# Kernel optimization log

Hardware: AMD Instinct MI355X
Metric: run time of the kernel (lower is better)

Reference implementation:

```python
import jax, jax.numpy as jnp
import numpy as np

BS, S, D, H, DFF, L = 8, 1024, 256, 8, 1024, 3
DK = D // H
NEG = -1e32


def setup_inputs() -> dict:
    key = jax.random.key(0)
    ks = jax.random.split(key, 10)
    r = lambda k, shp: jax.random.normal(k, shp, jnp.float32) * 0.02
    return {
        "q_embed_data": jax.random.normal(ks[0], (BS, S, D), jnp.float32),
        "qa_embed_data": jax.random.normal(ks[1], (BS, S, D), jnp.float32),
        "Wk": r(ks[2], (L, D, D)), "bk": jnp.zeros((L, D), jnp.float32),
        "Wv": r(ks[3], (L, D, D)), "bv": jnp.zeros((L, D), jnp.float32),
        "Wo": r(ks[4], (L, D, D)), "bo": jnp.zeros((L, D), jnp.float32),
        "gammas": r(ks[5], (L, H)),
        "ln1_g": jnp.ones((L, D), jnp.float32), "ln1_b": jnp.zeros((L, D), jnp.float32),
        "W1": r(ks[6], (L, D, DFF)), "b1": jnp.zeros((L, DFF), jnp.float32),
        "W2": r(ks[7], (L, DFF, D)), "b2": jnp.zeros((L, D), jnp.float32),
        "ln2_g": jnp.ones((L, D), jnp.float32), "ln2_b": jnp.zeros((L, D), jnp.float32),
    }


def _layernorm(x, g, b, eps=1e-5):
    mu = x.mean(-1, keepdims=True)
    var = ((x - mu) ** 2).mean(-1, keepdims=True)
    return (x - mu) * jax.lax.rsqrt(var + eps) * g + b


def _attn(xq, xk, xv, Wk, bk, Wv, bv, Wo, bo, gamma, mask, zero_pad):
    # kq_same=1: q and k both use k_linear
    bs = xq.shape[0]
    q = (xq @ Wk + bk).reshape(bs, S, H, DK).transpose(0, 2, 1, 3)  # bhsd
    k = (xk @ Wk + bk).reshape(bs, S, H, DK).transpose(0, 2, 1, 3)
    v = (xv @ Wv + bv).reshape(bs, S, H, DK).transpose(0, 2, 1, 3)
    scores = jnp.einsum('bhid,bhjd->bhij', q, k) / np.float32(np.sqrt(DK))
    mf = mask.astype(scores.dtype)
    # no-grad decay branch (detached in torch)
    p = jax.nn.softmax(jnp.where(mask, scores, NEG), axis=-1) * mf
    distcum = jnp.cumsum(p, axis=-1)
    disttot = p.sum(axis=-1, keepdims=True)
    idx = jnp.arange(S)
    pos = jnp.abs(idx[None, :] - idx[:, None]).astype(jnp.float32)[None, None]
    dist = jnp.sqrt(jnp.clip((disttot - distcum) * pos, 0.0, None))
    dist = jax.lax.stop_gradient(dist)
    g = -jax.nn.softplus(gamma)[None, :, None, None]  # (1,H,1,1)
    total_effect = jnp.clip(jnp.exp(dist * g), 1e-5, 1e5)
    scores = scores * total_effect
    attn = jax.nn.softmax(jnp.where(mask, scores, NEG), axis=-1)
    if zero_pad:
        attn = attn.at[:, :, 0, :].set(0.0)
    out = jnp.einsum('bhij,bhjd->bhid', attn, v)
    out = out.transpose(0, 2, 1, 3).reshape(bs, S, D)
    return out @ Wo + bo


def _block(i, xq, xk, xv, mask, zero_pad, apply_pos, P):
    Wk, bk, Wv, bv, Wo, bo, gam, l1g, l1b, W1, b1, W2, b2, l2g, l2b = [p[i] for p in P]
    q2 = _attn(xq, xk, xv, Wk, bk, Wv, bv, Wo, bo, gam, mask, zero_pad)
    x = _layernorm(xq + q2, l1g, l1b)
    if apply_pos:
        ff = jax.nn.relu(x @ W1 + b1) @ W2 + b2
        x = _layernorm(x + ff, l2g, l2b)
    return x


def _forward(q_embed_data, qa_embed_data, Wk, bk, Wv, bv, Wo, bo, gammas,
             ln1_g, ln1_b, W1, b1, W2, b2, ln2_g, ln2_b):
    P = (Wk, bk, Wv, bv, Wo, bo, gammas, ln1_g, ln1_b, W1, b1, W2, b2, ln2_g, ln2_b)
    tri_incl = jnp.tril(jnp.ones((S, S), bool))[None, None]       # mask=1: peek current+past
    tri_excl = jnp.tril(jnp.ones((S, S), bool), -1)[None, None]   # mask=0: strictly past
    x, y = q_embed_data, qa_embed_data
    # blocks_1 (n_blocks=1): mask=1, apply_pos=True, self-attn on y
    y = _block(0, y, y, y, tri_incl, False, True, P)
    # blocks_2 (2*n_blocks=2): alternate (mask=1, no FFN) / (mask=0, zero_pad, FFN, values=y)
    x = _block(1, x, x, x, tri_incl, False, False, P)
    x = _block(2, x, x, y, tri_excl, True, True, P)
    return x


def reference(q_embed_data, qa_embed_data, Wk, bk, Wv, bv, Wo, bo, gammas,
              ln1_g, ln1_b, W1, b1, W2, b2, ln2_g, ln2_b):
    return _forward(q_embed_data, qa_embed_data, Wk, bk, Wv, bv, Wo, bo, gammas,
                    ln1_g, ln1_b, W1, b1, W2, b2, ln2_g, ln2_b)
```

## Files before the change

### kernel.cpp

```cpp
#include <hip/hip_runtime.h>

typedef unsigned short u16;
typedef float f32x4 __attribute__((ext_vector_type(4)));
typedef __bf16 bf16x8 __attribute__((ext_vector_type(8)));
typedef u16 u16x8 __attribute__((ext_vector_type(8)));
typedef u16 u16x4 __attribute__((ext_vector_type(4)));

__device__ __forceinline__ u16 f2bf(float f) {
  union { float f; unsigned u; } v; v.f = f;
  unsigned r = (v.u + 0x7FFFu + ((v.u >> 16) & 1u)) >> 16;
  return (u16)r;
}
__device__ __forceinline__ float bf2f(u16 h) {
  union { unsigned u; float f; } v; v.u = ((unsigned)h) << 16;
  return v.f;
}
__device__ __forceinline__ unsigned cvtpk_bf16(float lo, float hi) {
  unsigned r;
  asm("v_cvt_pk_bf16_f32 %0, %1, %2" : "=v"(r) : "v"(lo), "v"(hi));
  return r;
}
__device__ __forceinline__ float wred_sum(float v) {
#pragma unroll
  for (int o = 32; o >= 1; o >>= 1) v += __shfl_xor(v, o);
  return v;
}

template <int RELU, int WF32, int WBF, int WVT>
__global__ __launch_bounds__(256) void gemm_kernel(
    const u16* __restrict__ A, const u16* __restrict__ Bt,
    const float* __restrict__ bias, float* __restrict__ C,
    u16* __restrict__ Cbf, int M, int N, int K) {
  __shared__ u16 As[64 * 64];
  __shared__ u16 Bs[64 * 64];
  const int tid = threadIdx.x;
  const int lane = tid & 63;
  const int w = tid >> 6;
  const int m0 = blockIdx.x * 64;
  const int n0 = blockIdx.y * 64;
  const int wr = (w >> 1) * 32;
  const int wc = (w & 1) * 32;
  const int l15 = lane & 15, hi = lane >> 4;

  f32x4 acc[2][2] = {};

  for (int k0 = 0; k0 < K; k0 += 64) {
#pragma unroll
    for (int rep = 0; rep < 2; ++rep) {
      int idx = tid + rep * 256;
      int row = idx >> 3, c8 = idx & 7;
      int cs = ((c8 ^ (row & 7)) << 3);
      __builtin_amdgcn_global_load_lds(
          (const __attribute__((address_space(1))) void*)(A + (size_t)(m0 + row) * K + k0 + cs),
          (__attribute__((address_space(3))) void*)(&As[idx * 8]), 16, 0, 0);
      __builtin_amdgcn_global_load_lds(
          (const __attribute__((address_space(1))) void*)(Bt + (size_t)(n0 + row) * K + k0 + cs),
          (__attribute__((address_space(3))) void*)(&Bs[idx * 8]), 16, 0, 0);
    }
    __syncthreads();
#pragma unroll
    for (int kk = 0; kk < 2; ++kk) {
      int kb = (kk * 32 + (hi << 3)) << 1;
      bf16x8 af[2], bfr[2];
#pragma unroll
      for (int mf = 0; mf < 2; ++mf) {
        int m = wr + mf * 16 + l15;
        af[mf] = *(const bf16x8*)((const char*)As + m * 128 + (kb ^ ((m & 7) << 4)));
      }
#pragma unroll
      for (int nf = 0; nf < 2; ++nf) {
        int n = wc + nf * 16 + l15;
        bfr[nf] = *(const bf16x8*)((const char*)Bs + n * 128 + (kb ^ ((n & 7) << 4)));
      }
#pragma unroll
      for (int mf = 0; mf < 2; ++mf)
#pragma unroll
        for (int nf = 0; nf < 2; ++nf)
          acc[mf][nf] = __builtin_amdgcn_mfma_f32_16x16x32_bf16(af[mf], bfr[nf], acc[mf][nf], 0, 0, 0);
    }
    __syncthreads();
  }

#pragma unroll
  for (int mf = 0; mf < 2; ++mf)
#pragma unroll
    for (int nf = 0; nf < 2; ++nf) {
      int col = n0 + wc + nf * 16 + l15;
      float bia = bias[col];
      u16x4 tv;
#pragma unroll
      for (int r = 0; r < 4; ++r) {
        int row = m0 + wr + mf * 16 + (hi << 2) + r;
        float val = acc[mf][nf][r] + bia;
        if (RELU) val = fmaxf(val, 0.f);
        if (WF32) C[(size_t)row * N + col] = val;
        if (WBF) Cbf[(size_t)row * N + col] = f2bf(val);
        if (WVT) tv[r] = f2bf(val);
      }
      if (WVT) {
        int row0 = m0 + wr + mf * 16 + (hi << 2);
        size_t addr = (((size_t)(row0 >> 10) * 8 + (col >> 5)) * 32 + (col & 31)) * 1024 + (row0 & 1023);
        *(u16x4*)(Cbf + addr) = tv;
      }
    }
}

template <int RELU>
__global__ __launch_bounds__(256) void gemm_w_kernel(
    const u16* __restrict__ A, const u16* __restrict__ Bt,
    const float* __restrict__ bias, u16* __restrict__ Cbf,
    int M, int N, int K) {
  __shared__ u16 As[64 * 64];
  __shared__ u16 Bs[128 * 64];
  const int tid = threadIdx.x;
  const int lane = tid & 63;
  const int w = tid >> 6;
  const int m0 = blockIdx.x * 64;
  const int n0 = blockIdx.y * 128;
  const int wr = (w >> 1) * 32;
  const int wc = (w & 1) * 64;
  const int l15 = lane & 15, hi = lane >> 4;

  f32x4 acc[2][4] = {};

  for (int k0 = 0; k0 < K; k0 += 64) {
#pragma unroll
    for (int rep = 0; rep < 2; ++rep) {
      int idx = tid + rep * 256;
      int row = idx >> 3, c8 = idx & 7;
      int cs = ((c8 ^ (row & 7)) << 3);
      __builtin_amdgcn_global_load_lds(
          (const __attribute__((address_space(1))) void*)(A + (size_t)(m0 + row) * K + k0 + cs),
          (__attribute__((address_space(3))) void*)(&As[idx * 8]), 16, 0, 0);
    }
#pragma unroll
    for (int rep = 0; rep < 4; ++rep) {
      int idx = tid + rep * 256;
      int row = idx >> 3, c8 = idx & 7;
      int cs = ((c8 ^ (row & 7)) << 3);
      __builtin_amdgcn_global_load_lds(
          (const __attribute__((address_space(1))) void*)(Bt + (size_t)(n0 + row) * K + k0 + cs),
          (__attribute__((address_space(3))) void*)(&Bs[idx * 8]), 16, 0, 0);
    }
    __syncthreads();
#pragma unroll
    for (int kk = 0; kk < 2; ++kk) {
      int kb = (kk * 32 + (hi << 3)) << 1;
      bf16x8 af[2], bfr[4];
#pragma unroll
      for (int mf = 0; mf < 2; ++mf) {
        int m = wr + mf * 16 + l15;
        af[mf] = *(const bf16x8*)((const char*)As + m * 128 + (kb ^ ((m & 7) << 4)));
      }
#pragma unroll
      for (int nf = 0; nf < 4; ++nf) {
        int n = wc + nf * 16 + l15;
        bfr[nf] = *(const bf16x8*)((const char*)Bs + n * 128 + (kb ^ ((n & 7) << 4)));
      }
#pragma unroll
      for (int mf = 0; mf < 2; ++mf)
#pragma unroll
        for (int nf = 0; nf < 4; ++nf)
          acc[mf][nf] = __builtin_amdgcn_mfma_f32_16x16x32_bf16(af[mf], bfr[nf], acc[mf][nf], 0, 0, 0);
    }
    __syncthreads();
  }

#pragma unroll
  for (int mf = 0; mf < 2; ++mf)
#pragma unroll
    for (int nf = 0; nf < 4; ++nf) {
      int col = n0 + wc + nf * 16 + l15;
      float bia = bias[col];
#pragma unroll
      for (int r = 0; r < 4; ++r) {
        int row = m0 + wr + mf * 16 + (hi << 2) + r;
        float val = acc[mf][nf][r] + bia;
        if (RELU) val = fmaxf(val, 0.f);
        Cbf[(size_t)row * N + col] = f2bf(val);
      }
    }
}

__global__ __launch_bounds__(256) void gemm_kv_kernel(
    const u16* __restrict__ A, const u16* __restrict__ Bt,
    const float* __restrict__ biasK, const float* __restrict__ biasV,
    u16* __restrict__ qkbf, u16* __restrict__ vT, int M, int N, int K) {
  __shared__ u16 As[64 * 64];
  __shared__ u16 Bs[128 * 64];
  const int tid = threadIdx.x;
  const int lane = tid & 63;
  const int w = tid >> 6;
  const int m0 = blockIdx.x * 64;
  const int n0 = blockIdx.y * 128;
  const int wr = (w >> 1) * 32;
  const int wc = (w & 1) * 64;
  const int l15 = lane & 15, hi = lane >> 4;

  f32x4 acc[2][4] = {};

  for (int k0 = 0; k0 < K; k0 += 64) {
#pragma unroll
    for (int rep = 0; rep < 2; ++rep) {
      int idx = tid + rep * 256;
      int row = idx >> 3, c8 = idx & 7;
      int cs = ((c8 ^ (row & 7)) << 3);
      __builtin_amdgcn_global_load_lds(
          (const __attribute__((address_space(1))) void*)(A + (size_t)(m0 + row) * K + k0 + cs),
          (__attribute__((address_space(3))) void*)(&As[idx * 8]), 16, 0, 0);
    }
#pragma unroll
    for (int rep = 0; rep < 4; ++rep) {
      int idx = tid + rep * 256;
      int row = idx >> 3, c8 = idx & 7;
      int cs = ((c8 ^ (row & 7)) << 3);
      __builtin_amdgcn_global_load_lds(
          (const __attribute__((address_space(1))) void*)(Bt + (size_t)(n0 + row) * K + k0 + cs),
          (__attribute__((address_space(3))) void*)(&Bs[idx * 8]), 16, 0, 0);
    }
    __syncthreads();
#pragma unroll
    for (int kk = 0; kk < 2; ++kk) {
      int kb = (kk * 32 + (hi << 3)) << 1;
      bf16x8 af[2], bfr[4];
#pragma unroll
      for (int mf = 0; mf < 2; ++mf) {
        int m = wr + mf * 16 + l15;
        af[mf] = *(const bf16x8*)((const char*)As + m * 128 + (kb ^ ((m & 7) << 4)));
      }
#pragma unroll
      for (int nf = 0; nf < 4; ++nf) {
        int n = wc + nf * 16 + l15;
        bfr[nf] = *(const bf16x8*)((const char*)Bs + n * 128 + (kb ^ ((n & 7) << 4)));
      }
#pragma unroll
      for (int mf = 0; mf < 2; ++mf)
#pragma unroll
        for (int nf = 0; nf < 4; ++nf)
          acc[mf][nf] = __builtin_amdgcn_mfma_f32_16x16x32_bf16(af[mf], bfr[nf], acc[mf][nf], 0, 0, 0);
    }
    __syncthreads();
  }

#pragma unroll
  for (int mf = 0; mf < 2; ++mf)
#pragma unroll
    for (int nf = 0; nf < 4; ++nf) {
      int col = n0 + wc + nf * 16 + l15;
      const bool isV = (col >= 256);
      float bia = isV ? biasV[col - 256] : biasK[col];
      u16x4 tv;
#pragma unroll
      for (int r = 0; r < 4; ++r) {
        int row = m0 + wr + mf * 16 + (hi << 2) + r;
        float val = acc[mf][nf][r] + bia;
        if (!isV) qkbf[(size_t)row * 256 + col] = f2bf(val);
        tv[r] = f2bf(val);
      }
      if (isV) {
        int row0 = m0 + wr + mf * 16 + (hi << 2);
        int vc = col - 256;
        size_t addr = (((size_t)(row0 >> 10) * 8 + (vc >> 5)) * 32 + (vc & 31)) * 1024 + (row0 & 1023);
        *(u16x4*)(vT + addr) = tv;
      }
    }
}

__global__ __launch_bounds__(256) void attn_mfma_kernel(
    const u16* __restrict__ qkbf, const u16* __restrict__ vT,
    u16* __restrict__ ao, const float* __restrict__ gam, int excl) {
  __shared__ float zbuf[4][16];
  __shared__ float z2buf[4][16];
  __shared__ float accbuf[8][4][64];

  const int lane = threadIdx.x & 63, w = threadIdx.x >> 6;
  const int qt = 63 - blockIdx.y;
  const int bh = blockIdx.x;
  const int b = bh >> 3, h = bh & 7;
  const int q0 = qt * 16;
  const int l15 = lane & 15, hi = lane >> 4;
  const int i = q0 + l15;
  const float LOG2E = 1.4426950408889634f;
  const float g2 = -log1pf(__expf(gam[h])) * LOG2E;
  const float cscale = 0.17677669529663687f * LOG2E;
  const float CLIP2 = -16.609640474436812f;

  const u16* kbase = qkbf + (size_t)b * 1024 * 256 + h * 32;
  const u16* vbase = vT + (size_t)bh * 32 * 1024;
  const bf16x8 qfrag = *(const bf16x8*)(kbase + (size_t)i * 256 + hi * 8);

  const int mylim = i - excl;
  const int jmax = q0 + 15 - excl;
  const int ntiles = (jmax >> 4) + 1;
  const int C = (ntiles + 3) >> 2;
  const int c0 = w * C;
  const int tEnd = (c0 + C < ntiles) ? (c0 + C) : ntiles;
  const int count = (tEnd > c0) ? (tEnd - c0) : 0;

  auto calc_l = [&](int t, float* l) {
    bf16x8 kf = *(const bf16x8*)(kbase + (size_t)(t * 16 + l15) * 256 + hi * 8);
    f32x4 sA = {};
    sA = __builtin_amdgcn_mfma_f32_16x16x32_bf16(kf, qfrag, sA, 0, 0, 0);
    l[0] = sA[0] * cscale; l[1] = sA[1] * cscale;
    l[2] = sA[2] * cscale; l[3] = sA[3] * cscale;
    if (t == ntiles - 1) {
      const int kb = t * 16 + hi * 4;
      l[0] = (kb + 0 <= mylim) ? l[0] : -1000.f;
      l[1] = (kb + 1 <= mylim) ? l[1] : -1000.f;
      l[2] = (kb + 2 <= mylim) ? l[2] : -1000.f;
      l[3] = (kb + 3 <= mylim) ? l[3] : -1000.f;
    }
  };

  float zacc = 0.f;
  for (int t = c0; t < tEnd; ++t) {
    float l[4]; calc_l(t, l);
    zacc += (exp2f(l[0]) + exp2f(l[1])) + (exp2f(l[2]) + exp2f(l[3]));
  }
  zacc += __shfl_xor(zacc, 16);
  zacc += __shfl_xor(zacc, 32);
  if (lane < 16) zbuf[w][lane] = zacc;
  __syncthreads();

  const float zc0 = zbuf[0][l15], zc1 = zbuf[1][l15];
  const float zc2 = zbuf[2][l15], zc3 = zbuf[3][l15];
  const float Z = zc0 + zc1 + zc2 + zc3;
  const float invZ = Z > 0.f ? 1.f / Z : 0.f;
  float prefix = 0.f;
  if (w > 0) prefix += zc0;
  if (w > 1) prefix += zc1;
  if (w > 2) prefix += zc2;

  float carry = prefix, z2 = 0.f;
  f32x4 acc0 = {}, acc1 = {};

  auto sm4 = [&](const float* l, int kb) -> uint2 {
    const float e0 = exp2f(l[0]), e1 = exp2f(l[1]);
    const float e2 = exp2f(l[2]), e3 = exp2f(l[3]);
    const float cA = e0 + e1, cB2 = cA + e2, cC = cB2 + e3;
    float vsc = cC;
    float tmp = __shfl_up(vsc, 16); if (hi >= 1) vsc += tmp;
    tmp = __shfl_up(vsc, 32); if (hi >= 2) vsc += tmp;
    const float exg = vsc - cC;
    const float tot = __shfl(vsc, l15 + 48);
    const float cb = carry + exg;
    carry += tot;
    const float posb = (float)(i - kb);
    const float r0 = (Z - (cb + e0)) * invZ;
    const float r1 = (Z - (cb + cA)) * invZ;
    const float r2 = (Z - (cb + cB2)) * invZ;
    const float r3 = (Z - (cb + cC)) * invZ;
    const float d20 = fmaxf(r0 * posb, 0.f);
    const float d21 = fmaxf(r1 * (posb - 1.f), 0.f);
    const float d22 = fmaxf(r2 * (posb - 2.f), 0.f);
    const float d23 = fmaxf(r3 * (posb - 3.f), 0.f);
    const float a0 = fmaxf(__builtin_amdgcn_sqrtf(d20) * g2, CLIP2);
    const float a1 = fmaxf(__builtin_amdgcn_sqrtf(d21) * g2, CLIP2);
    const float a2 = fmaxf(__builtin_amdgcn_sqrtf(d22) * g2, CLIP2);
    const float a3 = fmaxf(__builtin_amdgcn_sqrtf(d23) * g2, CLIP2);
    const float p0 = exp2f(l[0] * exp2f(a0));
    const float p1 = exp2f(l[1] * exp2f(a1));
    const float p2 = exp2f(l[2] * exp2f(a2));
    const float p3 = exp2f(l[3] * exp2f(a3));
    z2 += (p0 + p1) + (p2 + p3);
    uint2 r; r.x = cvtpk_bf16(p0, p1); r.y = cvtpk_bf16(p2, p3);
    return r;
  };

  const int Cp = (count + 1) & ~1;
  for (int tl = 0; tl < Cp; tl += 2) {
    const int t0 = c0 + tl, t1 = t0 + 1;
    float la[4], lb[4];
    calc_l(t0, la);
    const bool v1 = (tl + 1 < count);
    if (v1) calc_l(t1, lb);
    const int jb = t0 * 16;
    bf16x8 vf0 = *(const bf16x8*)(vbase + (size_t)l15 * 1024 + jb + hi * 8);
    bf16x8 vf1 = *(const bf16x8*)(vbase + (size_t)(16 + l15) * 1024 + jb + hi * 8);
    uint2 uA = sm4(la, t0 * 16 + hi * 4);
    uint2 uB = make_uint2(0u, 0u);
    if (v1) uB = sm4(lb, t1 * 16 + hi * 4);
    const int srcA = l15 + (((2 * hi) & 3) << 4);
    const int srcB = l15 + (((2 * hi + 1) & 3) << 4);
    unsigned a00 = (unsigned)__shfl((int)uA.x, srcA);
    unsigned a01 = (unsigned)__shfl((int)uB.x, srcA);
    unsigned a10 = (unsigned)__shfl((int)uA.y, srcA);
    unsigned a11 = (unsigned)__shfl((int)uB.y, srcA);
    unsigned b00 = (unsigned)__shfl((int)uA.x, srcB);
    unsigned b01 = (unsigned)__shfl((int)uB.x, srcB);
    unsigned b10 = (unsigned)__shfl((int)uA.y, srcB);
    unsigned b11 = (unsigned)__shfl((int)uB.y, srcB);
    const bool up = hi >= 2;
    union { unsigned u[4]; bf16x8 v; } pf;
    pf.u[0] = up ? a01 : a00;
    pf.u[1] = up ? a11 : a10;
    pf.u[2] = up ? b01 : b00;
    pf.u[3] = up ? b11 : b10;
    acc0 = __builtin_amdgcn_mfma_f32_16x16x32_bf16(vf0, pf.v, acc0, 0, 0, 0);
    acc1 = __builtin_amdgcn_mfma_f32_16x16x32_bf16(vf1, pf.v, acc1, 0, 0, 0);
  }

  z2 += __shfl_xor(z2, 16);
  z2 += __shfl_xor(z2, 32);
  if (lane < 16) z2buf[w][lane] = z2;
#pragma unroll
  for (int j = 0; j < 4; ++j) {
    accbuf[j][w][lane] = acc0[j];
    accbuf[4 + j][w][lane] = acc1[j];
  }
  __syncthreads();

  if (w == 0) {
    const float z2t = z2buf[0][l15] + z2buf[1][l15] + z2buf[2][l15] + z2buf[3][l15];
    const float inv2 = z2t > 0.f ? 1.f / z2t : 0.f;
    u16* aop = ao + ((size_t)(b * 1024 + i)) * 256 + h * 32;
    float s0[4], s1[4];
#pragma unroll
    for (int j = 0; j < 4; ++j) {
      s0[j] = (accbuf[j][0][lane] + accbuf[j][1][lane] + accbuf[j][2][lane] + accbuf[j][3][lane]) * inv2;
      s1[j] = (accbuf[4 + j][0][lane] + accbuf[4 + j][1][lane] + accbuf[4 + j][2][lane] + accbuf[4 + j][3][lane]) * inv2;
    }
    uint2 o0, o1;
    o0.x = cvtpk_bf16(s0[0], s0[1]); o0.y = cvtpk_bf16(s0[2], s0[3]);
    o1.x = cvtpk_bf16(s1[0], s1[1]); o1.y = cvtpk_bf16(s1[2], s1[3]);
    *(uint2*)(aop + hi * 4) = o0;
    *(uint2*)(aop + 16 + hi * 4) = o1;
  }
}

__global__ __launch_bounds__(256) void add_ln_kernel(
    const float* __restrict__ res, const u16* __restrict__ add,
    const float* __restrict__ g, const float* __restrict__ b,
    float* __restrict__ outf, u16* __restrict__ outb) {
  const int lane = threadIdx.x & 63, wid = threadIdx.x >> 6;
  const size_t row = (size_t)blockIdx.x * 4 + wid;
  const size_t base = row * 256 + lane * 4;
  float4 rv = *(const float4*)(res + base);
  u16x4 av = *(const u16x4*)(add + base);
  float x0 = rv.x + bf2f(av[0]), x1 = rv.y + bf2f(av[1]);
  float x2 = rv.z + bf2f(av[2]), x3 = rv.w + bf2f(av[3]);
  float sm = wred_sum(x0 + x1 + x2 + x3);
  float mu = sm * (1.f / 256.f);
  float d0 = x0 - mu, d1 = x1 - mu, d2 = x2 - mu, d3 = x3 - mu;
  float vs = wred_sum(d0 * d0 + d1 * d1 + d2 * d2 + d3 * d3);
  float rs = rsqrtf(vs * (1.f / 256.f) + 1e-5f);
  float4 gv = *(const float4*)(g + lane * 4);
  float4 bv = *(const float4*)(b + lane * 4);
  float o0 = d0 * rs * gv.x + bv.x;
  float o1 = d1 * rs * gv.y + bv.y;
  float o2 = d2 * rs * gv.z + bv.z;
  float o3 = d3 * rs * gv.w + bv.w;
  float4 ov = {o0, o1, o2, o3};
  *(float4*)(outf + base) = ov;
  u16x4 wv; wv[0] = f2bf(o0); wv[1] = f2bf(o1); wv[2] = f2bf(o2); wv[3] = f2bf(o3);
  *(u16x4*)(outb + base) = wv;
}

__global__ __launch_bounds__(256) void cast_bf_kernel(
    const float* __restrict__ in, u16* __restrict__ out) {
  size_t i = ((size_t)blockIdx.x * 256 + threadIdx.x) * 8;
  float4 a = *(const float4*)(in + i);
  float4 c = *(const float4*)(in + i + 4);
  u16x8 o;
  o[0] = f2bf(a.x); o[1] = f2bf(a.y); o[2] = f2bf(a.z); o[3] = f2bf(a.w);
  o[4] = f2bf(c.x); o[5] = f2bf(c.y); o[6] = f2bf(c.z); o[7] = f2bf(c.w);
  *(u16x8*)(out + i) = o;
}

__global__ __launch_bounds__(256) void transpose_cast_kernel(
    const float* __restrict__ W, u16* __restrict__ Wt, int K, int N,
    int dstStride) {
  __shared__ float t[32][33];
  const size_t lo = (size_t)blockIdx.z * K * N;
  const size_t lod = (size_t)blockIdx.z * dstStride;
  int n0 = blockIdx.x * 32, k0 = blockIdx.y * 32;
  int tx = threadIdx.x, ty = threadIdx.y;
#pragma unroll
  for (int r = 0; r < 32; r += 8)
    t[ty + r][tx] = W[lo + (size_t)(k0 + ty + r) * N + n0 + tx];
  __syncthreads();
#pragma unroll
  for (int r = 0; r < 32; r += 8)
    Wt[lod + (size_t)(n0 + ty + r) * K + k0 + tx] = f2bf(t[tx][ty + r]);
}

extern "C" void kernel_launch(void* const* d_in, const int* in_sizes, int n_in,
                              void* d_out, int out_size, void* d_ws,
                              size_t ws_size, hipStream_t stream) {
  const float* q_embed = (const float*)d_in[0];
  const float* qa_embed = (const float*)d_in[1];
  const float* Wk = (const float*)d_in[2];
  const float* bk = (const float*)d_in[3];
  const float* Wv = (const float*)d_in[4];
  const float* bv = (const float*)d_in[5];
  const float* Wo = (const float*)d_in[6];
  const float* bo = (const float*)d_in[7];
  const float* gammas = (const float*)d_in[8];
  const float* ln1_g = (const float*)d_in[9];
  const float* ln1_b = (const float*)d_in[10];
  const float* W1 = (const float*)d_in[11];
  const float* b1 = (const float*)d_in[12];
  const float* W2 = (const float*)d_in[13];
  const float* b2 = (const float*)d_in[14];
  const float* ln2_g = (const float*)d_in[15];
  const float* ln2_b = (const float*)d_in[16];

  const size_t ACT_F32 = (size_t)8192 * 256 * 4;
  const size_t ACT_BF = (size_t)8192 * 256 * 2;
  char* p = (char*)d_ws;
  auto carve = [&](size_t bytes) {
    void* r = (void*)p;
    p += (bytes + 255) & ~(size_t)255;
    return r;
  };
  float* yb = (float*)carve(ACT_F32);
  float* xb = (float*)carve(ACT_F32);
  u16* pofb = (u16*)carve(ACT_BF);
  u16* xbf = (u16*)carve(ACT_BF);
  u16* ybf = (u16*)carve(ACT_BF);
  u16* qkbf = (u16*)carve(ACT_BF);
  u16* vTb = (u16*)carve(ACT_BF);
  u16* aobf = (u16*)carve(ACT_BF);
  u16* hbf = (u16*)carve((size_t)8192 * 1024 * 2);
  u16* Wkvt = (u16*)carve((size_t)3 * 131072 * 2);
  u16* Wot = (u16*)carve((size_t)3 * 65536 * 2);
  u16* W1t = (u16*)carve((size_t)3 * 262144 * 2);
  u16* W2t = (u16*)carve((size_t)3 * 262144 * 2);

  dim3 tb(32, 8);
  transpose_cast_kernel<<<dim3(8, 8, 3), tb, 0, stream>>>(Wk, Wkvt, 256, 256, 131072);
  transpose_cast_kernel<<<dim3(8, 8, 3), tb, 0, stream>>>(Wv, Wkvt + 65536, 256, 256, 131072);
  transpose_cast_kernel<<<dim3(8, 8, 3), tb, 0, stream>>>(Wo, Wot, 256, 256, 65536);
  transpose_cast_kernel<<<dim3(32, 8, 3), tb, 0, stream>>>(W1, W1t, 256, 1024, 262144);
  transpose_cast_kernel<<<dim3(8, 32, 3), tb, 0, stream>>>(W2, W2t, 1024, 256, 262144);
  cast_bf_kernel<<<1024, 256, 0, stream>>>(q_embed, xbf);
  cast_bf_kernel<<<1024, 256, 0, stream>>>(qa_embed, ybf);

  const dim3 gP(128, 4), gKV(128, 4), gW1(128, 8);
  const dim3 gA(64, 64);

  gemm_kv_kernel<<<gKV, 256, 0, stream>>>(ybf, Wkvt, bk, bv, qkbf, vTb, 8192, 512, 256);
  attn_mfma_kernel<<<gA, 256, 0, stream>>>(qkbf, vTb, aobf, gammas, 0);
  gemm_kernel<0, 0, 1, 0><<<gP, 256, 0, stream>>>(aobf, Wot, bo, nullptr, pofb, 8192, 256, 256);
  add_ln_kernel<<<2048, 256, 0, stream>>>(qa_embed, pofb, ln1_g, ln1_b, yb, ybf);
  gemm_w_kernel<1><<<gW1, 256, 0, stream>>>(ybf, W1t, b1, hbf, 8192, 1024, 256);
  gemm_kernel<0, 0, 1, 0><<<gP, 256, 0, stream>>>(hbf, W2t, b2, nullptr, pofb, 8192, 256, 1024);
  add_ln_kernel<<<2048, 256, 0, stream>>>(yb, pofb, ln2_g, ln2_b, yb, ybf);

  gemm_kv_kernel<<<gKV, 256, 0, stream>>>(xbf, Wkvt + 131072, bk + 256, bv + 256, qkbf, vTb, 8192, 512, 256);
  attn_mfma_kernel<<<gA, 256, 0, stream>>>(qkbf, vTb, aobf, gammas + 8, 0);
  gemm_kernel<0, 0, 1, 0><<<gP, 256, 0, stream>>>(aobf, Wot + 65536, bo + 256, nullptr, pofb, 8192, 256, 256);
  add_ln_kernel<<<2048, 256, 0, stream>>>(q_embed, pofb, ln1_g + 256, ln1_b + 256, xb, xbf);

  gemm_kv_kernel<<<gKV, 256, 0, stream>>>(xbf, Wkvt + 262144, bk + 512, bv + 512, qkbf, vTb, 8192, 512, 256);
  gemm_kernel<0, 0, 0, 1><<<gP, 256, 0, stream>>>(ybf, Wkvt + 262144 + 65536, bv + 512, nullptr, vTb, 8192, 256, 256);
  attn_mfma_kernel<<<gA, 256, 0, stream>>>(qkbf, vTb, aobf, gammas + 16, 1);
  gemm_kernel<0, 0, 1, 0><<<gP, 256, 0, stream>>>(aobf, Wot + 131072, bo + 512, nullptr, pofb, 8192, 256, 256);
  add_ln_kernel<<<2048, 256, 0, stream>>>(xb, pofb, ln1_g + 512, ln1_b + 512, xb, xbf);
  gemm_w_kernel<1><<<gW1, 256, 0, stream>>>(xbf, W1t + 524288, b1 + 2048, hbf, 8192, 1024, 256);
  gemm_kernel<0, 0, 1, 0><<<gP, 256, 0, stream>>>(hbf, W2t + 524288, b2 + 512, nullptr, pofb, 8192, 256, 1024);
  add_ln_kernel<<<2048, 256, 0, stream>>>(xb, pofb, ln2_g + 512, ln2_b + 512, (float*)d_out, xbf);
}
```

Measured before the change: 313.7 us.

## Fuse output/FFN2 GEMMs with residual add and LayerNorm; merge prep kernels

Adds a gemm_ln kernel that computes a full 256-wide output row tile (32 rows per block) so the residual add and LayerNorm run in the GEMM epilogue. This removes the bf16 intermediate buffer round trip and the separate add_ln launches. The seven weight transpose/cast and embedding cast launches are merged into one prep kernel. The trade-offs are that each fused GEMM launches only 256 blocks with a large B tile in LDS, which may lower occupancy, and that variance is now computed as E[x^2]-mu^2 in a single pass.

```diff
diff --git a/kernel.cpp b/kernel.cpp
--- a/kernel.cpp
+++ b/kernel.cpp
@@ -11,26 +11,15 @@
   unsigned r = (v.u + 0x7FFFu + ((v.u >> 16) & 1u)) >> 16;
   return (u16)r;
 }
-__device__ __forceinline__ float bf2f(u16 h) {
-  union { unsigned u; float f; } v; v.u = ((unsigned)h) << 16;
-  return v.f;
-}
 __device__ __forceinline__ unsigned cvtpk_bf16(float lo, float hi) {
   unsigned r;
   asm("v_cvt_pk_bf16_f32 %0, %1, %2" : "=v"(r) : "v"(lo), "v"(hi));
   return r;
 }
-__device__ __forceinline__ float wred_sum(float v) {
-#pragma unroll
-  for (int o = 32; o >= 1; o >>= 1) v += __shfl_xor(v, o);
-  return v;
-}
-
-template <int RELU, int WF32, int WBF, int WVT>
-__global__ __launch_bounds__(256) void gemm_kernel(
+
+__global__ __launch_bounds__(256) void gemm_vt_kernel(
     const u16* __restrict__ A, const u16* __restrict__ Bt,
-    const float* __restrict__ bias, float* __restrict__ C,
-    u16* __restrict__ Cbf, int M, int N, int K) {
+    const float* __restrict__ bias, u16* __restrict__ vT, int M, int N, int K) {
   __shared__ u16 As[64 * 64];
   __shared__ u16 Bs[64 * 64];
   const int tid = threadIdx.x;
@@ -90,18 +79,12 @@
       u16x4 tv;
 #pragma unroll
       for (int r = 0; r < 4; ++r) {
-        int row = m0 + wr + mf * 16 + (hi << 2) + r;
         float val = acc[mf][nf][r] + bia;
-        if (RELU) val = fmaxf(val, 0.f);
-        if (WF32) C[(size_t)row * N + col] = val;
-        if (WBF) Cbf[(size_t)row * N + col] = f2bf(val);
-        if (WVT) tv[r] = f2bf(val);
-      }
-      if (WVT) {
-        int row0 = m0 + wr + mf * 16 + (hi << 2);
-        size_t addr = (((size_t)(row0 >> 10) * 8 + (col >> 5)) * 32 + (col & 31)) * 1024 + (row0 & 1023);
-        *(u16x4*)(Cbf + addr) = tv;
-      }
+        tv[r] = f2bf(val);
+      }
+      int row0 = m0 + wr + mf * 16 + (hi << 2);
+      size_t addr = (((size_t)(row0 >> 10) * 8 + (col >> 5)) * 32 + (col & 31)) * 1024 + (row0 & 1023);
+      *(u16x4*)(vT + addr) = tv;
     }
 }
 
@@ -264,6 +247,114 @@
         *(u16x4*)(vT + addr) = tv;
       }
     }
+}
+
+__global__ __launch_bounds__(256) void gemm_ln_kernel(
+    const u16* __restrict__ A, const u16* __restrict__ Bt,
+    const float* __restrict__ bias, const float* __restrict__ res,
+    const float* __restrict__ g, const float* __restrict__ b,
+    float* __restrict__ outf, u16* __restrict__ outb, int K) {
+  __shared__ u16 As[32 * 64];
+  __shared__ u16 Bs[256 * 64];
+  __shared__ float red[2][32][2];
+
+  const int tid = threadIdx.x;
+  const int lane = tid & 63;
+  const int w = tid >> 6;
+  const int rowgrp = w >> 1, colh = w & 1;
+  const int m0 = blockIdx.x * 32;
+  const int l15 = lane & 15, hi = lane >> 4;
+
+  f32x4 acc[8] = {};
+
+  for (int k0 = 0; k0 < K; k0 += 64) {
+    {
+      int row = tid >> 3, c8 = tid & 7;
+      int cs = ((c8 ^ (row & 7)) << 3);
+      __builtin_amdgcn_global_load_lds(
+          (const __attribute__((address_space(1))) void*)(A + (size_t)(m0 + row) * K + k0 + cs),
+          (__attribute__((address_space(3))) void*)(&As[tid * 8]), 16, 0, 0);
+    }
+#pragma unroll
+    for (int rep = 0; rep < 8; ++rep) {
+      int idx = tid + rep * 256;
+      int row = idx >> 3, c8 = idx & 7;
+      int cs = ((c8 ^ (row & 7)) << 3);
+      __builtin_amdgcn_global_load_lds(
+          (const __attribute__((address_space(1))) void*)(Bt + (size_t)row * K + k0 + cs),
+          (__attribute__((address_space(3))) void*)(&Bs[idx * 8]), 16, 0, 0);
+    }
+    __syncthreads();
+#pragma unroll
+    for (int kk = 0; kk < 2; ++kk) {
+      int kb = (kk * 32 + (hi << 3)) << 1;
+      int m = rowgrp * 16 + l15;
+      bf16x8 af = *(const bf16x8*)((const char*)As + m * 128 + (kb ^ ((m & 7) << 4)));
+      bf16x8 bfr[8];
+#pragma unroll
+      for (int nf = 0; nf < 8; ++nf) {
+        int n = colh * 128 + nf * 16 + l15;
+        bfr[nf] = *(const bf16x8*)((const char*)Bs + n * 128 + (kb ^ ((n & 7) << 4)));
+      }
+#pragma unroll
+      for (int nf = 0; nf < 8; ++nf)
+        acc[nf] = __builtin_amdgcn_mfma_f32_16x16x32_bf16(af, bfr[nf], acc[nf], 0, 0, 0);
+    }
+    __syncthreads();
+  }
+
+  const int rbase = m0 + rowgrp * 16 + hi * 4;
+  float s[4] = {0.f, 0.f, 0.f, 0.f}, ss[4] = {0.f, 0.f, 0.f, 0.f};
+#pragma unroll
+  for (int nf = 0; nf < 8; ++nf) {
+    int col = colh * 128 + nf * 16 + l15;
+    float bia = bias[col];
+#pragma unroll
+    for (int r = 0; r < 4; ++r) {
+      float v = acc[nf][r] + bia + res[(size_t)(rbase + r) * 256 + col];
+      acc[nf][r] = v;
+      s[r] += v;
+      ss[r] += v * v;
+    }
+  }
+#pragma unroll
+  for (int r = 0; r < 4; ++r) {
+#pragma unroll
+    for (int o = 1; o < 16; o <<= 1) {
+      s[r] += __shfl_xor(s[r], o);
+      ss[r] += __shfl_xor(ss[r], o);
+    }
+  }
+  if (l15 == 0) {
+#pragma unroll
+    for (int r = 0; r < 4; ++r) {
+      red[colh][rowgrp * 16 + hi * 4 + r][0] = s[r];
+      red[colh][rowgrp * 16 + hi * 4 + r][1] = ss[r];
+    }
+  }
+  __syncthreads();
+  float mu[4], rs[4];
+#pragma unroll
+  for (int r = 0; r < 4; ++r) {
+    int rr = rowgrp * 16 + hi * 4 + r;
+    float S = red[0][rr][0] + red[1][rr][0];
+    float SS = red[0][rr][1] + red[1][rr][1];
+    mu[r] = S * (1.f / 256.f);
+    float var = SS * (1.f / 256.f) - mu[r] * mu[r];
+    rs[r] = rsqrtf(var + 1e-5f);
+  }
+#pragma unroll
+  for (int nf = 0; nf < 8; ++nf) {
+    int col = colh * 128 + nf * 16 + l15;
+    float gv = g[col], bv = b[col];
+#pragma unroll
+    for (int r = 0; r < 4; ++r) {
+      float o = (acc[nf][r] - mu[r]) * rs[r] * gv + bv;
+      size_t addr = (size_t)(rbase + r) * 256 + col;
+      outf[addr] = o;
+      outb[addr] = f2bf(o);
+    }
+  }
 }
 
 __global__ __launch_bounds__(256) void attn_mfma_kernel(
@@ -428,60 +519,63 @@
   }
 }
 
-__global__ __launch_bounds__(256) void add_ln_kernel(
-    const float* __restrict__ res, const u16* __restrict__ add,
-    const float* __restrict__ g, const float* __restrict__ b,
-    float* __restrict__ outf, u16* __restrict__ outb) {
-  const int lane = threadIdx.x & 63, wid = threadIdx.x >> 6;
-  const size_t row = (size_t)blockIdx.x * 4 + wid;
-  const size_t base = row * 256 + lane * 4;
-  float4 rv = *(const float4*)(res + base);
-  u16x4 av = *(const u16x4*)(add + base);
-  float x0 = rv.x + bf2f(av[0]), x1 = rv.y + bf2f(av[1]);
-  float x2 = rv.z + bf2f(av[2]), x3 = rv.w + bf2f(av[3]);
-  float sm = wred_sum(x0 + x1 + x2 + x3);
-  float mu = sm * (1.f / 256.f);
-  float d0 = x0 - mu, d1 = x1 - mu, d2 = x2 - mu, d3 = x3 - mu;
-  float vs = wred_sum(d0 * d0 + d1 * d1 + d2 * d2 + d3 * d3);
-  float rs = rsqrtf(vs * (1.f / 256.f) + 1e-5f);
-  float4 gv = *(const float4*)(g + lane * 4);
-  float4 bv = *(const float4*)(b + lane * 4);
-  float o0 = d0 * rs * gv.x + bv.x;
-  float o1 = d1 * rs * gv.y + bv.y;
-  float o2 = d2 * rs * gv.z + bv.z;
-  float o3 = d3 * rs * gv.w + bv.w;
-  float4 ov = {o0, o1, o2, o3};
-  *(float4*)(outf + base) = ov;
-  u16x4 wv; wv[0] = f2bf(o0); wv[1] = f2bf(o1); wv[2] = f2bf(o2); wv[3] = f2bf(o3);
-  *(u16x4*)(outb + base) = wv;
-}
-
-__global__ __launch_bounds__(256) void cast_bf_kernel(
-    const float* __restrict__ in, u16* __restrict__ out) {
-  size_t i = ((size_t)blockIdx.x * 256 + threadIdx.x) * 8;
-  float4 a = *(const float4*)(in + i);
-  float4 c = *(const float4*)(in + i + 4);
-  u16x8 o;
-  o[0] = f2bf(a.x); o[1] = f2bf(a.y); o[2] = f2bf(a.z); o[3] = f2bf(a.w);
-  o[4] = f2bf(c.x); o[5] = f2bf(c.y); o[6] = f2bf(c.z); o[7] = f2bf(c.w);
-  *(u16x8*)(out + i) = o;
-}
-
-__global__ __launch_bounds__(256) void transpose_cast_kernel(
-    const float* __restrict__ W, u16* __restrict__ Wt, int K, int N,
-    int dstStride) {
+__global__ __launch_bounds__(256) void prep_kernel(
+    const float* __restrict__ Wk, const float* __restrict__ Wv,
+    const float* __restrict__ Wo, const float* __restrict__ W1,
+    const float* __restrict__ W2, const float* __restrict__ qe,
+    const float* __restrict__ qae, u16* __restrict__ Wkvt,
+    u16* __restrict__ Wot, u16* __restrict__ W1t, u16* __restrict__ W2t,
+    u16* __restrict__ xbf, u16* __restrict__ ybf) {
   __shared__ float t[32][33];
-  const size_t lo = (size_t)blockIdx.z * K * N;
-  const size_t lod = (size_t)blockIdx.z * dstStride;
-  int n0 = blockIdx.x * 32, k0 = blockIdx.y * 32;
-  int tx = threadIdx.x, ty = threadIdx.y;
-#pragma unroll
-  for (int r = 0; r < 32; r += 8)
-    t[ty + r][tx] = W[lo + (size_t)(k0 + ty + r) * N + n0 + tx];
-  __syncthreads();
-#pragma unroll
-  for (int r = 0; r < 32; r += 8)
-    Wt[lod + (size_t)(n0 + ty + r) * K + k0 + tx] = f2bf(t[tx][ty + r]);
+  const int bid = blockIdx.x;
+  const int tx = threadIdx.x, ty = threadIdx.y;
+
+  if (bid < 2112) {
+    const float* src; u16* dst;
+    int K, N, n0, k0;
+    size_t so, doff;
+    if (bid < 576) {
+      int wsel = bid / 192, r = bid % 192, z = r >> 6, tt = r & 63;
+      K = 256; N = 256;
+      n0 = (tt & 7) * 32; k0 = (tt >> 3) * 32;
+      so = (size_t)z * 65536;
+      if (wsel == 0)      { src = Wk; dst = Wkvt;        doff = (size_t)z * 131072; }
+      else if (wsel == 1) { src = Wv; dst = Wkvt + 65536; doff = (size_t)z * 131072; }
+      else                { src = Wo; dst = Wot;          doff = (size_t)z * 65536; }
+    } else if (bid < 1344) {
+      int r = bid - 576, z = r >> 8, tt = r & 255;
+      K = 256; N = 1024;
+      n0 = (tt & 31) * 32; k0 = (tt >> 5) * 32;
+      src = W1; dst = W1t;
+      so = (size_t)z * 262144; doff = (size_t)z * 262144;
+    } else {
+      int r = bid - 1344, z = r >> 8, tt = r & 255;
+      K = 1024; N = 256;
+      n0 = (tt & 7) * 32; k0 = (tt >> 3) * 32;
+      src = W2; dst = W2t;
+      so = (size_t)z * 262144; doff = (size_t)z * 262144;
+    }
+#pragma unroll
+    for (int r = 0; r < 32; r += 8)
+      t[ty + r][tx] = src[so + (size_t)(k0 + ty + r) * N + n0 + tx];
+    __syncthreads();
+#pragma unroll
+    for (int r = 0; r < 32; r += 8)
+      dst[doff + (size_t)(n0 + ty + r) * K + k0 + tx] = f2bf(t[tx][ty + r]);
+  } else {
+    int r = bid - 2112;
+    const float* in = (r < 1024) ? qe : qae;
+    u16* out = (r < 1024) ? xbf : ybf;
+    int rr = r & 1023;
+    int tid = ty * 32 + tx;
+    size_t i = ((size_t)rr * 256 + tid) * 8;
+    float4 a = *(const float4*)(in + i);
+    float4 c = *(const float4*)(in + i + 4);
+    u16x8 o;
+    o[0] = f2bf(a.x); o[1] = f2bf(a.y); o[2] = f2bf(a.z); o[3] = f2bf(a.w);
+    o[4] = f2bf(c.x); o[5] = f2bf(c.y); o[6] = f2bf(c.z); o[7] = f2bf(c.w);
+    *(u16x8*)(out + i) = o;
+  }
 }
 
 extern "C" void kernel_launch(void* const* d_in, const int* in_sizes, int n_in,
@@ -515,7 +609,6 @@
   };
   float* yb = (float*)carve(ACT_F32);
   float* xb = (float*)carve(ACT_F32);
-  u16* pofb = (u16*)carve(ACT_BF);
   u16* xbf = (u16*)carve(ACT_BF);
   u16* ybf = (u16*)carve(ACT_BF);
   u16* qkbf = (u16*)carve(ACT_BF);
@@ -527,37 +620,26 @@
   u16* W1t = (u16*)carve((size_t)3 * 262144 * 2);
   u16* W2t = (u16*)carve((size_t)3 * 262144 * 2);
 
-  dim3 tb(32, 8);
-  transpose_cast_kernel<<<dim3(8, 8, 3), tb, 0, stream>>>(Wk, Wkvt, 256, 256, 131072);
-  transpose_cast_kernel<<<dim3(8, 8, 3), tb, 0, stream>>>(Wv, Wkvt + 65536, 256, 256, 131072);
-  transpose_cast_kernel<<<dim3(8, 8, 3), tb, 0, stream>>>(Wo, Wot, 256, 256, 65536);
-  transpose_cast_kernel<<<dim3(32, 8, 3), tb, 0, stream>>>(W1, W1t, 256, 1024, 262144);
-  transpose_cast_kernel<<<dim3(8, 32, 3), tb, 0, stream>>>(W2, W2t, 1024, 256, 262144);
-  cast_bf_kernel<<<1024, 256, 0, stream>>>(q_embed, xbf);
-  cast_bf_kernel<<<1024, 256, 0, stream>>>(qa_embed, ybf);
-
-  const dim3 gP(128, 4), gKV(128, 4), gW1(128, 8);
+  prep_kernel<<<4160, dim3(32, 8), 0, stream>>>(
+      Wk, Wv, Wo, W1, W2, q_embed, qa_embed, Wkvt, Wot, W1t, W2t, xbf, ybf);
+
+  const dim3 gKV(128, 4), gW1(128, 8), gVT(128, 4);
   const dim3 gA(64, 64);
 
   gemm_kv_kernel<<<gKV, 256, 0, stream>>>(ybf, Wkvt, bk, bv, qkbf, vTb, 8192, 512, 256);
   attn_mfma_kernel<<<gA, 256, 0, stream>>>(qkbf, vTb, aobf, gammas, 0);
-  gemm_kernel<0, 0, 1, 0><<<gP, 256, 0, stream>>>(aobf, Wot, bo, nullptr, pofb, 8192, 256, 256);
-  add_ln_kernel<<<2048, 256, 0, stream>>>(qa_embed, pofb, ln1_g, ln1_b, yb, ybf);
+  gemm_ln_kernel<<<256, 256, 0, stream>>>(aobf, Wot, bo, qa_embed, ln1_g, ln1_b, yb, ybf, 256);
   gemm_w_kernel<1><<<gW1, 256, 0, stream>>>(ybf, W1t, b1, hbf, 8192, 1024, 256);
-  gemm_kernel<0, 0, 1, 0><<<gP, 256, 0, stream>>>(hbf, W2t, b2, nullptr, pofb, 8192, 256, 1024);
-  add_ln_kernel<<<2048, 256, 0, stream>>>(yb, pofb, ln2_g, ln2_b, yb, ybf);
+  gemm_ln_kernel<<<256, 256, 0, stream>>>(hbf, W2t, b2, yb, ln2_g, ln2_b, yb, ybf, 1024);
 
   gemm_kv_kernel<<<gKV, 256, 0, stream>>>(xbf, Wkvt + 131072, bk + 256, bv + 256, qkbf, vTb, 8192, 512, 256);
   attn_mfma_kernel<<<gA, 256, 0, stream>>>(qkbf, vTb, aobf, gammas + 8, 0);
-  gemm_kernel<0, 0, 1, 0><<<gP, 256, 0, stream>>>(aobf, Wot + 65536, bo + 256, nullptr, pofb, 8192, 256, 256);
-  add_ln_kernel<<<2048, 256, 0, stream>>>(q_embed, pofb, ln1_g + 256, ln1_b + 256, xb, xbf);
+  gemm_ln_kernel<<<256, 256, 0, stream>>>(aobf, Wot + 65536, bo + 256, q_embed, ln1_g + 256, ln1_b + 256, xb, xbf, 256);
 
   gemm_kv_kernel<<<gKV, 256, 0, stream>>>(xbf, Wkvt + 262144, bk + 512, bv + 512, qkbf, vTb, 8192, 512, 256);
-  gemm_kernel<0, 0, 0, 1><<<gP, 256, 0, stream>>>(ybf, Wkvt + 262144 + 65536, bv + 512, nullptr, vTb, 8192, 256, 256);
+  gemm_vt_kernel<<<gVT, 256, 0, stream>>>(ybf, Wkvt + 262144 + 65536, bv + 512, vTb, 8192, 256, 256);
   attn_mfma_kernel<<<gA, 256, 0, stream>>>(qkbf, vTb, aobf, gammas + 16, 1);
-  gemm_kernel<0, 0, 1, 0><<<gP, 256, 0, stream>>>(aobf, Wot + 131072, bo + 512, nullptr, pofb, 8192, 256, 256);
-  add_ln_kernel<<<2048, 256, 0, stream>>>(xb, pofb, ln1_g + 512, ln1_b + 512, xb, xbf);
+  gemm_ln_kernel<<<256, 256, 0, stream>>>(aobf, Wot + 131072, bo + 512, xb, ln1_g + 512, ln1_b + 512, xb, xbf, 256);
   gemm_w_kernel<1><<<gW1, 256, 0, stream>>>(xbf, W1t + 524288, b1 + 2048, hbf, 8192, 1024, 256);
-  gemm_kernel<0, 0, 1, 0><<<gP, 256, 0, stream>>>(hbf, W2t + 524288, b2 + 512, nullptr, pofb, 8192, 256, 1024);
-  add_ln_kernel<<<2048, 256, 0, stream>>>(xb, pofb, ln2_g + 512, ln2_b + 512, (float*)d_out, xbf);
-}
+  gemm_ln_kernel<<<256, 256, 0, stream>>>(hbf, W2t + 524288, b2 + 512, xb, ln2_g + 512, ln2_b + 512, (float*)d_out, xbf, 1024);
+}
```

Measured after the change: 307.5 us. 1.02x faster.
